# Kernel tuning notes

Measured on AMD Instinct MI355X. Metric: run time of the kernel, lower is better.

The kernel has to match this reference:

```python
import jax, jax.numpy as jnp
import numpy as np
import math

D_MODEL, N_HEADS, D_FF = 512, 8, 2048
B, S = 2, 2048
EPS = 1e-6


def _layernorm(x, g, b):
    mu = jnp.mean(x, axis=-1, keepdims=True)
    var = jnp.mean((x - mu) ** 2, axis=-1, keepdims=True)
    return (x - mu) * jax.lax.rsqrt(var + EPS) * g + b


def setup_inputs() -> dict:
    key = jax.random.key(0)
    ks = jax.random.split(key, 16)
    sd = 1.0 / math.sqrt(D_MODEL)
    return {
        "x": jax.random.normal(ks[0], (B, S, D_MODEL), jnp.float32),
        "sensor_weights": jax.random.uniform(ks[1], (B, S, 4), jnp.float32),
        "mask": jnp.ones((1, 1, S, S), jnp.int32),
        "Wq": jax.random.normal(ks[2], (D_MODEL, D_MODEL), jnp.float32) * sd,
        "Wk": jax.random.normal(ks[3], (D_MODEL, D_MODEL), jnp.float32) * sd,
        "Wv": jax.random.normal(ks[4], (D_MODEL, D_MODEL), jnp.float32) * sd,
        "Wo": jax.random.normal(ks[5], (D_MODEL, D_MODEL), jnp.float32) * sd,
        "bo": jnp.zeros((D_MODEL,), jnp.float32),
        "sensor_attention": jnp.ones((N_HEADS, 4), jnp.float32),  # init = ones
        "temporal_bias": jax.random.normal(ks[6], (1, N_HEADS, 1, 1), jnp.float32) * 0.02,
        "ln1_g": jnp.ones((D_MODEL,), jnp.float32),
        "ln1_b": jnp.zeros((D_MODEL,), jnp.float32),
        "ln2_g": jnp.ones((D_MODEL,), jnp.float32),
        "ln2_b": jnp.zeros((D_MODEL,), jnp.float32),
        "W1": jax.random.normal(ks[7], (D_MODEL, D_FF), jnp.float32) * sd,
        "b1": jnp.zeros((D_FF,), jnp.float32),
        "W2": jax.random.normal(ks[8], (D_FF, D_MODEL), jnp.float32) * (1.0 / math.sqrt(D_FF)),
        "b2": jnp.zeros((D_MODEL,), jnp.float32),
    }


def reference(x, sensor_weights, mask, Wq, Wk, Wv, Wo, bo, sensor_attention,
              temporal_bias, ln1_g, ln1_b, ln2_g, ln2_b, W1, b1, W2, b2):
    b, s, d = x.shape
    h = temporal_bias.shape[1]
    dk = d // h
    scale = math.sqrt(dk)

    # [b, h, s, dk]
    q = (x @ Wq).reshape(b, s, h, dk).transpose(0, 2, 1, 3)
    k = (x @ Wk).reshape(b, s, h, dk).transpose(0, 2, 1, 3)
    v = (x @ Wv).reshape(b, s, h, dk).transpose(0, 2, 1, 3)

    scores = jnp.einsum('bhqd,bhkd->bhqk', q, k) / scale  # [b,h,s,s]
    scores = scores + temporal_bias
    # sensor bias: [h,4] x [b,s,4] -> [b,h,s], added per query row
    sensor_bias = jnp.einsum('hf,bsf->bhs', sensor_attention, sensor_weights)
    scores = scores + sensor_bias[..., None]
    scores = jnp.where(mask == 0, jnp.asarray(-1e9, scores.dtype), scores)

    attn = jax.nn.softmax(scores, axis=-1)
    ctx = jnp.einsum('bhqk,bhkd->bhqd', attn, v)
    ctx = ctx.transpose(0, 2, 1, 3).reshape(b, s, d)
    attn_out = ctx @ Wo + bo

    x1 = _layernorm(x + attn_out, ln1_g, ln1_b)
    ff = jax.nn.gelu(x1 @ W1 + b1, approximate=False) @ W2 + b2
    x2 = _layernorm(x1 + ff, ln2_g, ln2_b)
    return x2, attn
```

## Files before the change

### kernel.cpp

```cpp
#include <hip/hip_runtime.h>
#include <cstdint>
#include <cstddef>

#define S_LEN 2048
#define DM 512
#define NH 8
#define DK 64
#define DFF 2048
#define BATCH 2
#define NROWS (BATCH*S_LEN)
#define BHN (BATCH*NH)

#define MASKED_L2 (-1.4426950408889634e9f)
#define QSCALE 0.18033688011112042f

typedef __attribute__((ext_vector_type(8))) _Float16 f16x8;
typedef __attribute__((ext_vector_type(4))) float f32x4;

#define MFMA(a,b,c) __builtin_amdgcn_mfma_f32_16x16x32_f16(a,b,c,0,0,0)

__device__ __forceinline__ unsigned short f2h(float x){
  union{ _Float16 h; unsigned short u; } c; c.h = (_Float16)x; return c.u;
}
__device__ __forceinline__ int sw64(int r, int c){
  return r*64 + ((((c>>3) ^ r) & 7)<<3) + (c&7);
}
__device__ __forceinline__ int sw32(int r, int c){
  return r*32 + ((((c>>3) ^ r) & 3)<<3) + (c&7);
}

__global__ __launch_bounds__(256) void prep_kernel(
    const float* __restrict__ x, const int* __restrict__ mask,
    const float* __restrict__ Wq, const float* __restrict__ Wk,
    const float* __restrict__ Wv, const float* __restrict__ Wo,
    const float* __restrict__ W1, const float* __restrict__ W2,
    unsigned short* __restrict__ xb,
    unsigned short* __restrict__ wqT, unsigned short* __restrict__ wkT,
    unsigned short* __restrict__ wvT, unsigned short* __restrict__ woT,
    unsigned short* __restrict__ w1T, unsigned short* __restrict__ w2T,
    unsigned* __restrict__ maskw)
{
  const int z = blockIdx.y;
  const int t = blockIdx.x;
  const int tid = threadIdx.x;
  if (z < 6){
    const float* W; unsigned short* WT; int K, N;
    switch(z){
      case 0: W=Wq; WT=wqT; K=512;  N=512;  break;
      case 1: W=Wk; WT=wkT; K=512;  N=512;  break;
      case 2: W=Wv; WT=wvT; K=512;  N=512;  break;
      case 3: W=Wo; WT=woT; K=512;  N=512;  break;
      case 4: W=W1; WT=w1T; K=512;  N=2048; break;
      default:W=W2; WT=w2T; K=2048; N=512;  break;
    }
    const int ntiles = N>>5, ktiles = K>>5;
    if (t >= ntiles*ktiles) return;
    const int kt = t / ntiles, nt = t - kt*ntiles;
    __shared__ float tile[32][33];
    const int tx = tid & 31, ty = tid >> 5;
    #pragma unroll
    for (int i=0;i<4;i++){
      int r = ty + i*8;
      tile[r][tx] = W[(size_t)(kt*32 + r)*N + nt*32 + tx];
    }
    __syncthreads();
    #pragma unroll
    for (int i=0;i<4;i++){
      int r = ty + i*8;
      WT[(size_t)(nt*32 + r)*K + kt*32 + tx] = f2h(tile[tx][r]);
    }
  } else if (z == 6){
    size_t base = (size_t)t*2048 + (size_t)tid*8;
    float4 a = *(const float4*)(x + base);
    float4 b = *(const float4*)(x + base + 4);
    union{ unsigned short h[8]; uint4 v; } pk;
    pk.h[0]=f2h(a.x); pk.h[1]=f2h(a.y); pk.h[2]=f2h(a.z); pk.h[3]=f2h(a.w);
    pk.h[4]=f2h(b.x); pk.h[5]=f2h(b.y); pk.h[6]=f2h(b.z); pk.h[7]=f2h(b.w);
    *(uint4*)(xb + base) = pk.v;
  } else {
    if (t >= 512) return;
    const int gid = t*256 + tid;
    const int row = gid >> 6, w = gid & 63;
    const int4* mp = (const int4*)(mask + (size_t)row*2048 + w*32);
    unsigned word = 0;
    #pragma unroll
    for (int j=0;j<8;j++){
      int4 v = mp[j];
      word |= (unsigned)(v.x!=0) << (j*4+0);
      word |= (unsigned)(v.y!=0) << (j*4+1);
      word |= (unsigned)(v.z!=0) << (j*4+2);
      word |= (unsigned)(v.w!=0) << (j*4+3);
    }
    maskw[gid] = word;
  }
}

template<int KD, int EPI>
__global__ __launch_bounds__(256) void gemm_kernel(
    const unsigned short* __restrict__ A,
    const unsigned short* __restrict__ BT0,
    const unsigned short* __restrict__ BT1,
    const unsigned short* __restrict__ BT2,
    const float* __restrict__ bias,
    const float* __restrict__ resid,
    float* __restrict__ outf,
    unsigned short* __restrict__ ob0,
    unsigned short* __restrict__ ob1,
    unsigned short* __restrict__ ob2)
{
  const unsigned short* BT = BT0;
  unsigned short* outb = ob0;
  float scale = 1.0f;
  if (EPI == 0){
    const int z = blockIdx.z;
    if (z == 0) scale = QSCALE;
    else if (z == 1){ BT = BT1; outb = ob1; }
    else            { BT = BT2; outb = ob2; }
  }
  const int m0 = blockIdx.x*64, n0 = blockIdx.y*64;
  const int tid = threadIdx.x;
  const int wid = tid>>6, l = tid&63, quad = l>>4, lc = l&15;
  const int wm = wid&1, wn = wid>>1;
  __shared__ __align__(16) unsigned short As[2][64*32];
  __shared__ __align__(16) unsigned short Bs[2][64*32];
  const int sr = tid>>2, sc = (tid&3)*8;
  const unsigned short* Ap = A  + (size_t)(m0+sr)*KD + sc;
  const unsigned short* Bp = BT + (size_t)(n0+sr)*KD + sc;
  {
    uint4 va = *(const uint4*)Ap;
    uint4 vb = *(const uint4*)Bp;
    *(uint4*)&As[0][sw32(sr,sc)] = va;
    *(uint4*)&Bs[0][sw32(sr,sc)] = vb;
  }
  f32x4 acc00={0,0,0,0}, acc01={0,0,0,0}, acc10={0,0,0,0}, acc11={0,0,0,0};
  const int ar0 = wm*32 + lc, ar1 = wm*32 + 16 + lc;
  const int br0 = wn*32 + lc, br1 = wn*32 + 16 + lc;
  __syncthreads();
  constexpr int NK = KD/32;
  for (int kk=0; kk<NK; kk++){
    const int cur = kk & 1;
    if (kk+1 < NK){
      uint4 va = *(const uint4*)(Ap + (size_t)(kk+1)*32);
      uint4 vb = *(const uint4*)(Bp + (size_t)(kk+1)*32);
      *(uint4*)&As[cur^1][sw32(sr,sc)] = va;
      *(uint4*)&Bs[cur^1][sw32(sr,sc)] = vb;
    }
    f16x8 a0 = *(const f16x8*)&As[cur][sw32(ar0, quad*8)];
    f16x8 a1 = *(const f16x8*)&As[cur][sw32(ar1, quad*8)];
    f16x8 b0 = *(const f16x8*)&Bs[cur][sw32(br0, quad*8)];
    f16x8 b1 = *(const f16x8*)&Bs[cur][sw32(br1, quad*8)];
    acc00 = MFMA(a0,b0,acc00);
    acc01 = MFMA(a0,b1,acc01);
    acc10 = MFMA(a1,b0,acc10);
    acc11 = MFMA(a1,b1,acc11);
    __syncthreads();
  }
  f32x4 accs[2][2] = {{acc00,acc01},{acc10,acc11}};
  #pragma unroll
  for (int mt=0;mt<2;mt++){
    #pragma unroll
    for (int nt=0;nt<2;nt++){
      f32x4 v = accs[mt][nt];
      const int col  = n0 + wn*32 + nt*16 + lc;
      const int row0 = m0 + wm*32 + mt*16 + quad*4;
      #pragma unroll
      for (int r=0;r<4;r++){
        const int row = row0 + r;
        const float val = v[r];
        if (EPI == 0){
          const int h = col>>6, d = col&63, b = row>>11, s = row&2047;
          outb[(((size_t)(b*NH + h))*S_LEN + s)*DK + d] = f2h(val*scale);
        } else if (EPI == 1){
          const size_t idx = (size_t)row*DM + col;
          outf[idx] = val + bias[col] + resid[idx];
        } else {
          const float xx = val + bias[col];
          const float gg = 0.5f*xx*(1.0f + erff(xx*0.70710678118654752f));
          outb[(size_t)row*DFF + col] = f2h(gg);
        }
      }
    }
  }
}

__global__ __launch_bounds__(256) void kml_kernel(
    const unsigned short* __restrict__ qw,
    const unsigned short* __restrict__ kw,
    const unsigned* __restrict__ maskw,
    float* __restrict__ m_out, float* __restrict__ li_out)
{
  const int bh = blockIdx.y, q0 = blockIdx.x*64;
  const int tid = threadIdx.x, wid = tid>>6, l = tid&63, quad = l>>4, lc = l&15;
  __shared__ __align__(16) unsigned short Qs[64*64];
  __shared__ __align__(16) unsigned short Ks[2][64*64];
  const unsigned short* qbase = qw + ((size_t)bh*S_LEN + q0)*DK;
  const unsigned short* kbase = kw + (size_t)bh*S_LEN*DK;
  #pragma unroll
  for (int i=0;i<2;i++){
    const int idx = tid + i*256, r = idx>>3, c0 = (idx&7)*8;
    *(uint4*)&Qs[sw64(r,c0)]    = *(const uint4*)(qbase + (size_t)r*DK + c0);
    *(uint4*)&Ks[0][sw64(r,c0)] = *(const uint4*)(kbase + (size_t)r*DK + c0);
  }
  __syncthreads();
  f16x8 aQ0, aQ1;
  {
    const int r = wid*16 + lc;
    aQ0 = *(const f16x8*)&Qs[sw64(r, quad*8)];
    aQ1 = *(const f16x8*)&Qs[sw64(r, 32 + quad*8)];
  }
  float m[4]  = {-3e38f,-3e38f,-3e38f,-3e38f};
  float ls[4] = {0.f,0.f,0.f,0.f};
  const int rowb = q0 + wid*16 + quad*4;
  for (int c=0;c<32;c++){
    const int cur = c & 1;
    if (c+1 < 32){
      #pragma unroll
      for (int i=0;i<2;i++){
        const int idx = tid + i*256, r = idx>>3, c0 = (idx&7)*8;
        *(uint4*)&Ks[cur^1][sw64(r,c0)] =
          *(const uint4*)(kbase + ((size_t)(c+1)*64 + r)*DK + c0);
      }
    }
    uint2 mw[4];
    #pragma unroll
    for (int r=0;r<4;r++)
      mw[r] = *(const uint2*)(maskw + (size_t)(rowb+r)*64 + c*2);
    float sv[4][4];
    #pragma unroll
    for (int nt=0; nt<4; nt++){
      f16x8 b0 = *(const f16x8*)&Ks[cur][sw64(nt*16+lc, quad*8)];
      f16x8 b1 = *(const f16x8*)&Ks[cur][sw64(nt*16+lc, 32+quad*8)];
      f32x4 s = {0,0,0,0};
      s = MFMA(aQ0, b0, s);
      s = MFMA(aQ1, b1, s);
      const int sh = (nt&1)*16 + lc;
      #pragma unroll
      for (int r=0;r<4;r++){
        const unsigned w = (nt<2) ? mw[r].x : mw[r].y;
        sv[nt][r] = ((w>>sh)&1u) ? s[r] : MASKED_L2;
      }
    }
    #pragma unroll
    for (int r=0;r<4;r++){
      const float mc = fmaxf(fmaxf(sv[0][r],sv[1][r]), fmaxf(sv[2][r],sv[3][r]));
      const float m2 = fmaxf(m[r], mc);
      ls[r] = ls[r]*__builtin_exp2f(m[r]-m2)
            + __builtin_exp2f(sv[0][r]-m2) + __builtin_exp2f(sv[1][r]-m2)
            + __builtin_exp2f(sv[2][r]-m2) + __builtin_exp2f(sv[3][r]-m2);
      m[r] = m2;
    }
    __syncthreads();
  }
  #pragma unroll
  for (int o=1;o<16;o<<=1){
    #pragma unroll
    for (int r=0;r<4;r++){
      const float mo = __shfl_xor(m[r], o, 64);
      const float lo = __shfl_xor(ls[r], o, 64);
      const float m2 = fmaxf(m[r], mo);
      ls[r] = ls[r]*__builtin_exp2f(m[r]-m2) + lo*__builtin_exp2f(mo-m2);
      m[r] = m2;
    }
  }
  if (lc == 0){
    const size_t rowg = (size_t)bh*S_LEN + rowb;
    #pragma unroll
    for (int r=0;r<4;r++){
      m_out[rowg+r]  = m[r];
      li_out[rowg+r] = 1.0f/ls[r];
    }
  }
}

__global__ __launch_bounds__(256) void kattn_kernel(
    const unsigned short* __restrict__ qw,
    const unsigned short* __restrict__ kw,
    const unsigned short* __restrict__ vw,
    const unsigned* __restrict__ maskw,
    const float* __restrict__ m_in,
    const float* __restrict__ li_in,
    float* __restrict__ attn,
    unsigned short* __restrict__ ctx)
{
  const int bh = blockIdx.y, q0 = blockIdx.x*64;
  const int tid = threadIdx.x, wid = tid>>6, l = tid&63, quad = l>>4, lc = l&15;
  __shared__ __align__(16) unsigned short Qs[64*64];
  __shared__ __align__(16) unsigned short Ks[2][64*64];
  __shared__ __align__(16) unsigned short Vs[2][64*64];
  __shared__ __align__(16) unsigned short Ps[4][16*64];
  const unsigned short* qbase = qw + ((size_t)bh*S_LEN + q0)*DK;
  const unsigned short* kbase = kw + (size_t)bh*S_LEN*DK;
  const unsigned short* vbase = vw + (size_t)bh*S_LEN*DK;
  #pragma unroll
  for (int i=0;i<2;i++){
    const int idx = tid + i*256, r = idx>>3, c0 = (idx&7)*8;
    *(uint4*)&Qs[sw64(r,c0)]    = *(const uint4*)(qbase + (size_t)r*DK + c0);
    *(uint4*)&Ks[0][sw64(r,c0)] = *(const uint4*)(kbase + (size_t)r*DK + c0);
    union { uint4 u; unsigned short h[8]; } U;
    U.u = *(const uint4*)(vbase + (size_t)r*DK + c0);
    #pragma unroll
    for (int j=0;j<8;j++) Vs[0][sw64(c0+j, r)] = U.h[j];
  }
  __syncthreads();
  f16x8 aQ0, aQ1;
  {
    const int r = wid*16 + lc;
    aQ0 = *(const f16x8*)&Qs[sw64(r, quad*8)];
    aQ1 = *(const f16x8*)&Qs[sw64(r, 32 + quad*8)];
  }
  const int rowb = q0 + wid*16 + quad*4;
  float mr[4], li[4];
  #pragma unroll
  for (int r=0;r<4;r++){
    mr[r] = m_in[(size_t)bh*S_LEN + rowb + r];
    li[r] = li_in[(size_t)bh*S_LEN + rowb + r];
  }
  f32x4 O0={0,0,0,0}, O1={0,0,0,0}, O2={0,0,0,0}, O3={0,0,0,0};
  float* attnbase = attn + (size_t)bh*S_LEN*S_LEN;
  unsigned short* myP = &Ps[wid][0];
  for (int c=0;c<32;c++){
    const int cur = c & 1;
    if (c+1 < 32){
      #pragma unroll
      for (int i=0;i<2;i++){
        const int idx = tid + i*256, r = idx>>3, c0 = (idx&7)*8;
        *(uint4*)&Ks[cur^1][sw64(r,c0)] =
          *(const uint4*)(kbase + ((size_t)(c+1)*64 + r)*DK + c0);
        union { uint4 u; unsigned short h[8]; } U;
        U.u = *(const uint4*)(vbase + ((size_t)(c+1)*64 + r)*DK + c0);
        #pragma unroll
        for (int j=0;j<8;j++) Vs[cur^1][sw64(c0+j, r)] = U.h[j];
      }
    }
    uint2 mw[4];
    #pragma unroll
    for (int r=0;r<4;r++)
      mw[r] = *(const uint2*)(maskw + (size_t)(rowb+r)*64 + c*2);
    #pragma unroll
    for (int nt=0; nt<4; nt++){
      f16x8 b0 = *(const f16x8*)&Ks[cur][sw64(nt*16+lc, quad*8)];
      f16x8 b1 = *(const f16x8*)&Ks[cur][sw64(nt*16+lc, 32+quad*8)];
      f32x4 s = {0,0,0,0};
      s = MFMA(aQ0, b0, s);
      s = MFMA(aQ1, b1, s);
      const int sh = (nt&1)*16 + lc;
      #pragma unroll
      for (int r=0;r<4;r++){
        const unsigned w = (nt<2) ? mw[r].x : mw[r].y;
        const float se = ((w>>sh)&1u) ? s[r] : MASKED_L2;
        const float p  = __builtin_exp2f(se - mr[r]) * li[r];
        __builtin_nontemporal_store(p,
          attnbase + (size_t)(rowb+r)*S_LEN + (size_t)c*64 + nt*16 + lc);
        myP[sw64(quad*4+r, nt*16+lc)] = f2h(p);
      }
    }
    #pragma unroll
    for (int ks=0; ks<2; ks++){
      f16x8 aP = *(const f16x8*)&myP[sw64(lc, ks*32 + quad*8)];
      f16x8 v0 = *(const f16x8*)&Vs[cur][sw64( 0+lc, ks*32+quad*8)];
      f16x8 v1 = *(const f16x8*)&Vs[cur][sw64(16+lc, ks*32+quad*8)];
      f16x8 v2 = *(const f16x8*)&Vs[cur][sw64(32+lc, ks*32+quad*8)];
      f16x8 v3 = *(const f16x8*)&Vs[cur][sw64(48+lc, ks*32+quad*8)];
      O0 = MFMA(aP, v0, O0);
      O1 = MFMA(aP, v1, O1);
      O2 = MFMA(aP, v2, O2);
      O3 = MFMA(aP, v3, O3);
    }
    __syncthreads();
  }
  const int b = bh>>3, h = bh&7;
  f32x4 Os[4] = {O0,O1,O2,O3};
  #pragma unroll
  for (int nt=0; nt<4; nt++){
    #pragma unroll
    for (int r=0;r<4;r++){
      ctx[((size_t)b*S_LEN + rowb + r)*DM + h*DK + nt*16 + lc] = f2h(Os[nt][r]);
    }
  }
}

__global__ __launch_bounds__(256) void ln_kernel(
    const float* __restrict__ in, const float* __restrict__ g,
    const float* __restrict__ b, float* __restrict__ outf,
    unsigned short* __restrict__ outb)
{
  const int row = blockIdx.x*4 + (threadIdx.x>>6);
  const int l = threadIdx.x & 63;
  const float* p = in + (size_t)row*DM + l*8;
  float4 v0 = *(const float4*)p;
  float4 v1 = *(const float4*)(p+4);
  float vals[8] = {v0.x,v0.y,v0.z,v0.w,v1.x,v1.y,v1.z,v1.w};
  float s = 0.f, q = 0.f;
  #pragma unroll
  for (int j=0;j<8;j++){ s += vals[j]; q += vals[j]*vals[j]; }
  #pragma unroll
  for (int o=1;o<64;o<<=1){ s += __shfl_xor(s,o,64); q += __shfl_xor(q,o,64); }
  const float mu = s*(1.0f/DM);
  const float var = q*(1.0f/DM) - mu*mu;
  const float rs = rsqrtf(var + 1e-6f);
  const float* gp = g + l*8;
  const float* bp = b + l*8;
  float4 g0 = *(const float4*)gp, g1 = *(const float4*)(gp+4);
  float4 bb0 = *(const float4*)bp, bb1 = *(const float4*)(bp+4);
  float gv[8] = {g0.x,g0.y,g0.z,g0.w,g1.x,g1.y,g1.z,g1.w};
  float bv[8] = {bb0.x,bb0.y,bb0.z,bb0.w,bb1.x,bb1.y,bb1.z,bb1.w};
  float ov[8];
  #pragma unroll
  for (int j=0;j<8;j++) ov[j] = (vals[j]-mu)*rs*gv[j] + bv[j];
  float* op = outf + (size_t)row*DM + l*8;
  *(float4*)op     = make_float4(ov[0],ov[1],ov[2],ov[3]);
  *(float4*)(op+4) = make_float4(ov[4],ov[5],ov[6],ov[7]);
  if (outb){
    union{ unsigned short h[8]; uint4 v; } pk;
    #pragma unroll
    for (int j=0;j<8;j++) pk.h[j] = f2h(ov[j]);
    *(uint4*)(outb + (size_t)row*DM + l*8) = pk.v;
  }
}

extern "C" void kernel_launch(void* const* d_in, const int* in_sizes, int n_in,
                              void* d_out, int out_size, void* d_ws, size_t ws_size,
                              hipStream_t stream)
{
  const float* x    = (const float*)d_in[0];
  const int*   mask = (const int*)d_in[2];
  const float* Wq   = (const float*)d_in[3];
  const float* Wk   = (const float*)d_in[4];
  const float* Wv   = (const float*)d_in[5];
  const float* Wo   = (const float*)d_in[6];
  const float* bo   = (const float*)d_in[7];
  const float* ln1g = (const float*)d_in[10];
  const float* ln1b = (const float*)d_in[11];
  const float* ln2g = (const float*)d_in[12];
  const float* ln2b = (const float*)d_in[13];
  const float* W1   = (const float*)d_in[14];
  const float* b1   = (const float*)d_in[15];
  const float* W2   = (const float*)d_in[16];
  const float* b2   = (const float*)d_in[17];

  float* x2_out   = (float*)d_out;
  float* attn_out = x2_out + (size_t)NROWS*DM;

  char* p = (char*)d_ws;
  auto alloc = [&](size_t bytes)->char*{
    char* r = p; p += (bytes + 255) & ~(size_t)255; return r;
  };
  unsigned short* xb   = (unsigned short*)alloc((size_t)NROWS*DM*2);
  unsigned short* wqT  = (unsigned short*)alloc(512*512*2);
  unsigned short* wkT  = (unsigned short*)alloc(512*512*2);
  unsigned short* wvT  = (unsigned short*)alloc(512*512*2);
  unsigned short* woT  = (unsigned short*)alloc(512*512*2);
  unsigned short* w1T  = (unsigned short*)alloc(2048*512*2);
  unsigned short* w2T  = (unsigned short*)alloc(512*2048*2);
  unsigned short* q_ws = (unsigned short*)alloc((size_t)BHN*S_LEN*DK*2);
  unsigned short* k_ws = (unsigned short*)alloc((size_t)BHN*S_LEN*DK*2);
  unsigned short* v_ws = (unsigned short*)alloc((size_t)BHN*S_LEN*DK*2);
  unsigned*       maskw= (unsigned*)alloc((size_t)S_LEN*64*4);
  float*          m_ws = (float*)alloc((size_t)BHN*S_LEN*4);
  float*          li_ws= (float*)alloc((size_t)BHN*S_LEN*4);
  unsigned short* ctxb = (unsigned short*)alloc((size_t)NROWS*DM*2);
  float*          yv   = (float*)alloc((size_t)NROWS*DM*4);
  float*          x1f  = (float*)alloc((size_t)NROWS*DM*4);
  unsigned short* x1b  = (unsigned short*)alloc((size_t)NROWS*DM*2);
  unsigned short* hb   = (unsigned short*)alloc((size_t)NROWS*DFF*2);
  float*          zv   = (float*)alloc((size_t)NROWS*DM*4);

  prep_kernel<<<dim3(1024,8), 256, 0, stream>>>(
      x, mask, Wq, Wk, Wv, Wo, W1, W2,
      xb, wqT, wkT, wvT, woT, w1T, w2T, maskw);

  gemm_kernel<512,0><<<dim3(64,8,3), 256, 0, stream>>>(
      xb, wqT, wkT, wvT, nullptr, nullptr, nullptr, q_ws, k_ws, v_ws);

  kml_kernel<<<dim3(32,16), 256, 0, stream>>>(q_ws, k_ws, maskw, m_ws, li_ws);

  kattn_kernel<<<dim3(32,16), 256, 0, stream>>>(
      q_ws, k_ws, v_ws, maskw, m_ws, li_ws, attn_out, ctxb);

  gemm_kernel<512,1><<<dim3(64,8), 256, 0, stream>>>(
      ctxb, woT, nullptr, nullptr, bo, x, yv, nullptr, nullptr, nullptr);

  ln_kernel<<<1024, 256, 0, stream>>>(yv, ln1g, ln1b, x1f, x1b);

  gemm_kernel<512,2><<<dim3(64,32), 256, 0, stream>>>(
      x1b, w1T, nullptr, nullptr, b1, nullptr, nullptr, hb, nullptr, nullptr);

  gemm_kernel<2048,1><<<dim3(64,8), 256, 0, stream>>>(
      hb, w2T, nullptr, nullptr, b2, x1f, zv, nullptr, nullptr, nullptr);

  ln_kernel<<<1024, 256, 0, stream>>>(zv, ln2g, ln2b, x2_out, nullptr);

  (void)in_sizes; (void)n_in; (void)out_size; (void)ws_size;
}
```

Measured before the change: 542.7 us.

## Fuse attention passes, add direct-to-LDS GEMM with larger tiles, pre-transpose V

The two attention kernels (row max/sum pass and probability/context pass) become one kernel. It computes the softmax statistics first, then recomputes the scores to write the attention matrix and the context, and it reads K and a pre-transposed V straight from global memory instead of staging them in shared memory. The GEMMs are replaced by a templated kernel with larger tiles that loads global data directly into LDS, and Q/K/V come from one concatenated weight matrix. This cuts launches and shared-memory traffic, at the cost of a single-buffered GEMM pipeline with no overlap, unswizzled LDS reads that may hit bank conflicts, and an extra V transpose kernel.

```diff
diff --git a/kernel.cpp b/kernel.cpp
--- a/kernel.cpp
+++ b/kernel.cpp
@@ -25,8 +25,11 @@
 __device__ __forceinline__ int sw64(int r, int c){
   return r*64 + ((((c>>3) ^ r) & 7)<<3) + (c&7);
 }
-__device__ __forceinline__ int sw32(int r, int c){
-  return r*32 + ((((c>>3) ^ r) & 3)<<3) + (c&7);
+
+typedef const __attribute__((address_space(1))) uint32_t* gas1;
+typedef __attribute__((address_space(3))) uint32_t* las3;
+__device__ __forceinline__ void gl_lds16(const unsigned short* g, unsigned short* l){
+  __builtin_amdgcn_global_load_lds((gas1)(const void*)g, (las3)(void*)l, 16, 0, 0);
 }
 
 __global__ __launch_bounds__(256) void prep_kernel(
@@ -35,9 +38,8 @@
     const float* __restrict__ Wv, const float* __restrict__ Wo,
     const float* __restrict__ W1, const float* __restrict__ W2,
     unsigned short* __restrict__ xb,
-    unsigned short* __restrict__ wqT, unsigned short* __restrict__ wkT,
-    unsigned short* __restrict__ wvT, unsigned short* __restrict__ woT,
-    unsigned short* __restrict__ w1T, unsigned short* __restrict__ w2T,
+    unsigned short* __restrict__ wqkvT, unsigned short* __restrict__ woT,
+    unsigned short* __restrict__ w1T,   unsigned short* __restrict__ w2T,
     unsigned* __restrict__ maskw)
 {
   const int z = blockIdx.y;
@@ -46,12 +48,12 @@
   if (z < 6){
     const float* W; unsigned short* WT; int K, N;
     switch(z){
-      case 0: W=Wq; WT=wqT; K=512;  N=512;  break;
-      case 1: W=Wk; WT=wkT; K=512;  N=512;  break;
-      case 2: W=Wv; WT=wvT; K=512;  N=512;  break;
-      case 3: W=Wo; WT=woT; K=512;  N=512;  break;
-      case 4: W=W1; WT=w1T; K=512;  N=2048; break;
-      default:W=W2; WT=w2T; K=2048; N=512;  break;
+      case 0: W=Wq; WT=wqkvT;            K=512;  N=512;  break;
+      case 1: W=Wk; WT=wqkvT+512*512;    K=512;  N=512;  break;
+      case 2: W=Wv; WT=wqkvT+2*512*512;  K=512;  N=512;  break;
+      case 3: W=Wo; WT=woT;              K=512;  N=512;  break;
+      case 4: W=W1; WT=w1T;              K=512;  N=2048; break;
+      default:W=W2; WT=w2T;              K=2048; N=512;  break;
     }
     const int ntiles = N>>5, ktiles = K>>5;
     if (t >= ntiles*ktiles) return;
@@ -95,130 +97,156 @@
   }
 }
 
-template<int KD, int EPI>
-__global__ __launch_bounds__(256) void gemm_kernel(
+template<int BM, int BN, int KD, int EPI>
+__global__ __launch_bounds__(256) void gemm2(
     const unsigned short* __restrict__ A,
-    const unsigned short* __restrict__ BT0,
-    const unsigned short* __restrict__ BT1,
-    const unsigned short* __restrict__ BT2,
+    const unsigned short* __restrict__ BT,
     const float* __restrict__ bias,
     const float* __restrict__ resid,
     float* __restrict__ outf,
-    unsigned short* __restrict__ ob0,
-    unsigned short* __restrict__ ob1,
-    unsigned short* __restrict__ ob2)
-{
-  const unsigned short* BT = BT0;
-  unsigned short* outb = ob0;
-  float scale = 1.0f;
-  if (EPI == 0){
-    const int z = blockIdx.z;
-    if (z == 0) scale = QSCALE;
-    else if (z == 1){ BT = BT1; outb = ob1; }
-    else            { BT = BT2; outb = ob2; }
-  }
-  const int m0 = blockIdx.x*64, n0 = blockIdx.y*64;
-  const int tid = threadIdx.x;
-  const int wid = tid>>6, l = tid&63, quad = l>>4, lc = l&15;
-  const int wm = wid&1, wn = wid>>1;
-  __shared__ __align__(16) unsigned short As[2][64*32];
-  __shared__ __align__(16) unsigned short Bs[2][64*32];
-  const int sr = tid>>2, sc = (tid&3)*8;
-  const unsigned short* Ap = A  + (size_t)(m0+sr)*KD + sc;
-  const unsigned short* Bp = BT + (size_t)(n0+sr)*KD + sc;
-  {
-    uint4 va = *(const uint4*)Ap;
-    uint4 vb = *(const uint4*)Bp;
-    *(uint4*)&As[0][sw32(sr,sc)] = va;
-    *(uint4*)&Bs[0][sw32(sr,sc)] = vb;
-  }
-  f32x4 acc00={0,0,0,0}, acc01={0,0,0,0}, acc10={0,0,0,0}, acc11={0,0,0,0};
-  const int ar0 = wm*32 + lc, ar1 = wm*32 + 16 + lc;
-  const int br0 = wn*32 + lc, br1 = wn*32 + 16 + lc;
-  __syncthreads();
-  constexpr int NK = KD/32;
-  for (int kk=0; kk<NK; kk++){
-    const int cur = kk & 1;
-    if (kk+1 < NK){
-      uint4 va = *(const uint4*)(Ap + (size_t)(kk+1)*32);
-      uint4 vb = *(const uint4*)(Bp + (size_t)(kk+1)*32);
-      *(uint4*)&As[cur^1][sw32(sr,sc)] = va;
-      *(uint4*)&Bs[cur^1][sw32(sr,sc)] = vb;
-    }
-    f16x8 a0 = *(const f16x8*)&As[cur][sw32(ar0, quad*8)];
-    f16x8 a1 = *(const f16x8*)&As[cur][sw32(ar1, quad*8)];
-    f16x8 b0 = *(const f16x8*)&Bs[cur][sw32(br0, quad*8)];
-    f16x8 b1 = *(const f16x8*)&Bs[cur][sw32(br1, quad*8)];
-    acc00 = MFMA(a0,b0,acc00);
-    acc01 = MFMA(a0,b1,acc01);
-    acc10 = MFMA(a1,b0,acc10);
-    acc11 = MFMA(a1,b1,acc11);
+    unsigned short* __restrict__ outq,
+    unsigned short* __restrict__ outk,
+    unsigned short* __restrict__ outv)
+{
+  constexpr int WGM = (BM >= 128) ? 2 : 1;
+  constexpr int WGN = 4 / WGM;
+  constexpr int WTM = BM / WGM;
+  constexpr int WTN = BN / WGN;
+  constexpr int MT = WTM / 16;
+  constexpr int NT = WTN / 16;
+  constexpr int NKS = KD / 32;
+  constexpr int AISS = (BM*4)/256;
+  constexpr int BISS = (BN*4)/256;
+  __shared__ __align__(16) unsigned short As[BM*32];
+  __shared__ __align__(16) unsigned short Bs[BN*32];
+  const int tid = threadIdx.x, wid = tid>>6, l = tid&63, quad = l>>4, lc = l&15;
+  const int m0 = blockIdx.x*BM, n0 = blockIdx.y*BN;
+  const int wm = (WGM==2) ? (wid&1) : 0;
+  const int wn = (WGM==2) ? (wid>>1) : wid;
+  f32x4 acc[MT][NT] = {};
+  for (int kk=0; kk<NKS; kk++){
+    #pragma unroll
+    for (int i=0;i<AISS;i++){
+      const int ch = i*256 + tid;
+      gl_lds16(A + (size_t)(m0 + (ch>>2))*KD + kk*32 + (ch&3)*8,
+               &As[(i*256 + wid*64)*8]);
+    }
+    #pragma unroll
+    for (int i=0;i<BISS;i++){
+      const int ch = i*256 + tid;
+      gl_lds16(BT + (size_t)(n0 + (ch>>2))*KD + kk*32 + (ch&3)*8,
+               &Bs[(i*256 + wid*64)*8]);
+    }
     __syncthreads();
-  }
-  f32x4 accs[2][2] = {{acc00,acc01},{acc10,acc11}};
-  #pragma unroll
-  for (int mt=0;mt<2;mt++){
-    #pragma unroll
-    for (int nt=0;nt<2;nt++){
-      f32x4 v = accs[mt][nt];
-      const int col  = n0 + wn*32 + nt*16 + lc;
-      const int row0 = m0 + wm*32 + mt*16 + quad*4;
+    f16x8 af[MT], bf[NT];
+    #pragma unroll
+    for (int i=0;i<MT;i++)
+      af[i] = *(const f16x8*)&As[(wm*WTM + i*16 + lc)*32 + quad*8];
+    #pragma unroll
+    for (int j=0;j<NT;j++)
+      bf[j] = *(const f16x8*)&Bs[(wn*WTN + j*16 + lc)*32 + quad*8];
+    #pragma unroll
+    for (int i=0;i<MT;i++)
+      #pragma unroll
+      for (int j=0;j<NT;j++)
+        acc[i][j] = MFMA(af[i], bf[j], acc[i][j]);
+    __syncthreads();
+  }
+  #pragma unroll
+  for (int i=0;i<MT;i++){
+    const int row0 = m0 + wm*WTM + i*16 + quad*4;
+    #pragma unroll
+    for (int j=0;j<NT;j++){
+      const int col = n0 + wn*WTN + j*16 + lc;
+      f32x4 v = acc[i][j];
       #pragma unroll
       for (int r=0;r<4;r++){
         const int row = row0 + r;
         const float val = v[r];
         if (EPI == 0){
-          const int h = col>>6, d = col&63, b = row>>11, s = row&2047;
-          outb[(((size_t)(b*NH + h))*S_LEN + s)*DK + d] = f2h(val*scale);
+          const int z = col>>9, cw = col&511, h = cw>>6, d = cw&63;
+          const int b = row>>11, s = row&2047;
+          unsigned short* dst = (z==0)?outq:(z==1)?outk:outv;
+          const float sc = (z==0)?QSCALE:1.0f;
+          dst[(((size_t)(b*NH + h))*S_LEN + s)*DK + d] = f2h(val*sc);
         } else if (EPI == 1){
           const size_t idx = (size_t)row*DM + col;
           outf[idx] = val + bias[col] + resid[idx];
         } else {
           const float xx = val + bias[col];
           const float gg = 0.5f*xx*(1.0f + erff(xx*0.70710678118654752f));
-          outb[(size_t)row*DFF + col] = f2h(gg);
+          outq[(size_t)row*DFF + col] = f2h(gg);
         }
       }
     }
   }
 }
 
-__global__ __launch_bounds__(256) void kml_kernel(
+__global__ __launch_bounds__(256) void vtrans_kernel(
+    const unsigned short* __restrict__ v, unsigned short* __restrict__ vt)
+{
+  __shared__ unsigned short t[64][66];
+  const int bh = blockIdx.y, s0 = blockIdx.x*64;
+  const int tid = threadIdx.x;
+  #pragma unroll
+  for (int i=0;i<2;i++){
+    const int idx = tid + i*256;
+    const int row = idx>>3, col = (idx&7)*8;
+    *(uint4*)&t[row][col] =
+      *(const uint4*)(v + ((size_t)bh*S_LEN + s0 + row)*DK + col);
+  }
+  __syncthreads();
+  #pragma unroll
+  for (int i=0;i<2;i++){
+    const int idx = tid + i*256;
+    const int d = idx>>3, sc = (idx&7)*8;
+    union{ unsigned short h[8]; uint4 u; } pk;
+    #pragma unroll
+    for (int j=0;j<8;j++) pk.h[j] = t[sc+j][d];
+    *(uint4*)(vt + ((size_t)bh*DK + d)*S_LEN + s0 + sc) = pk.u;
+  }
+}
+
+__global__ __launch_bounds__(256) void attn_fused(
     const unsigned short* __restrict__ qw,
     const unsigned short* __restrict__ kw,
+    const unsigned short* __restrict__ vt,
     const unsigned* __restrict__ maskw,
-    float* __restrict__ m_out, float* __restrict__ li_out)
-{
-  const int bh = blockIdx.y, q0 = blockIdx.x*64;
+    float* __restrict__ attn,
+    unsigned short* __restrict__ ctx)
+{
+  const int bh = blockIdx.y;
   const int tid = threadIdx.x, wid = tid>>6, l = tid&63, quad = l>>4, lc = l&15;
-  __shared__ __align__(16) unsigned short Qs[64*64];
-  __shared__ __align__(16) unsigned short Ks[2][64*64];
-  const unsigned short* qbase = qw + ((size_t)bh*S_LEN + q0)*DK;
-  const unsigned short* kbase = kw + (size_t)bh*S_LEN*DK;
-  #pragma unroll
-  for (int i=0;i<2;i++){
-    const int idx = tid + i*256, r = idx>>3, c0 = (idx&7)*8;
-    *(uint4*)&Qs[sw64(r,c0)]    = *(const uint4*)(qbase + (size_t)r*DK + c0);
-    *(uint4*)&Ks[0][sw64(r,c0)] = *(const uint4*)(kbase + (size_t)r*DK + c0);
-  }
-  __syncthreads();
-  f16x8 aQ0, aQ1;
-  {
-    const int r = wid*16 + lc;
-    aQ0 = *(const f16x8*)&Qs[sw64(r, quad*8)];
-    aQ1 = *(const f16x8*)&Qs[sw64(r, 32 + quad*8)];
-  }
+  const int q0 = blockIdx.x*64 + wid*16;
+  __shared__ __align__(16) unsigned short Pbuf[4][16*64];
+  unsigned short* myP = Pbuf[wid];
+  const unsigned short* qb = qw + ((size_t)bh*S_LEN + q0)*DK;
+  const unsigned short* kb = kw + (size_t)bh*S_LEN*DK;
+  const unsigned short* vb = vt + (size_t)bh*DK*S_LEN;
+  const f16x8 aQ0 = *(const f16x8*)(qb + (size_t)lc*DK + quad*8);
+  const f16x8 aQ1 = *(const f16x8*)(qb + (size_t)lc*DK + 32 + quad*8);
+  const int rowb = q0 + quad*4;
+
   float m[4]  = {-3e38f,-3e38f,-3e38f,-3e38f};
   float ls[4] = {0.f,0.f,0.f,0.f};
-  const int rowb = q0 + wid*16 + quad*4;
+
+  f16x8 nb0[4], nb1[4];
+  #pragma unroll
+  for (int nt=0;nt<4;nt++){
+    const unsigned short* kp = kb + (size_t)(nt*16+lc)*DK;
+    nb0[nt] = *(const f16x8*)(kp + quad*8);
+    nb1[nt] = *(const f16x8*)(kp + 32 + quad*8);
+  }
   for (int c=0;c<32;c++){
-    const int cur = c & 1;
+    f16x8 cb0[4], cb1[4];
+    #pragma unroll
+    for (int nt=0;nt<4;nt++){ cb0[nt]=nb0[nt]; cb1[nt]=nb1[nt]; }
     if (c+1 < 32){
       #pragma unroll
-      for (int i=0;i<2;i++){
-        const int idx = tid + i*256, r = idx>>3, c0 = (idx&7)*8;
-        *(uint4*)&Ks[cur^1][sw64(r,c0)] =
-          *(const uint4*)(kbase + ((size_t)(c+1)*64 + r)*DK + c0);
+      for (int nt=0;nt<4;nt++){
+        const unsigned short* kp = kb + (size_t)((c+1)*64 + nt*16+lc)*DK;
+        nb0[nt] = *(const f16x8*)(kp + quad*8);
+        nb1[nt] = *(const f16x8*)(kp + 32 + quad*8);
       }
     }
     uint2 mw[4];
@@ -227,12 +255,10 @@
       mw[r] = *(const uint2*)(maskw + (size_t)(rowb+r)*64 + c*2);
     float sv[4][4];
     #pragma unroll
-    for (int nt=0; nt<4; nt++){
-      f16x8 b0 = *(const f16x8*)&Ks[cur][sw64(nt*16+lc, quad*8)];
-      f16x8 b1 = *(const f16x8*)&Ks[cur][sw64(nt*16+lc, 32+quad*8)];
+    for (int nt=0;nt<4;nt++){
       f32x4 s = {0,0,0,0};
-      s = MFMA(aQ0, b0, s);
-      s = MFMA(aQ1, b1, s);
+      s = MFMA(aQ0, cb0[nt], s);
+      s = MFMA(aQ1, cb1[nt], s);
       const int sh = (nt&1)*16 + lc;
       #pragma unroll
       for (int r=0;r<4;r++){
@@ -249,7 +275,6 @@
             + __builtin_exp2f(sv[2][r]-m2) + __builtin_exp2f(sv[3][r]-m2);
       m[r] = m2;
     }
-    __syncthreads();
   }
   #pragma unroll
   for (int o=1;o<16;o<<=1){
@@ -262,84 +287,22 @@
       m[r] = m2;
     }
   }
-  if (lc == 0){
-    const size_t rowg = (size_t)bh*S_LEN + rowb;
-    #pragma unroll
-    for (int r=0;r<4;r++){
-      m_out[rowg+r]  = m[r];
-      li_out[rowg+r] = 1.0f/ls[r];
-    }
-  }
-}
-
-__global__ __launch_bounds__(256) void kattn_kernel(
-    const unsigned short* __restrict__ qw,
-    const unsigned short* __restrict__ kw,
-    const unsigned short* __restrict__ vw,
-    const unsigned* __restrict__ maskw,
-    const float* __restrict__ m_in,
-    const float* __restrict__ li_in,
-    float* __restrict__ attn,
-    unsigned short* __restrict__ ctx)
-{
-  const int bh = blockIdx.y, q0 = blockIdx.x*64;
-  const int tid = threadIdx.x, wid = tid>>6, l = tid&63, quad = l>>4, lc = l&15;
-  __shared__ __align__(16) unsigned short Qs[64*64];
-  __shared__ __align__(16) unsigned short Ks[2][64*64];
-  __shared__ __align__(16) unsigned short Vs[2][64*64];
-  __shared__ __align__(16) unsigned short Ps[4][16*64];
-  const unsigned short* qbase = qw + ((size_t)bh*S_LEN + q0)*DK;
-  const unsigned short* kbase = kw + (size_t)bh*S_LEN*DK;
-  const unsigned short* vbase = vw + (size_t)bh*S_LEN*DK;
-  #pragma unroll
-  for (int i=0;i<2;i++){
-    const int idx = tid + i*256, r = idx>>3, c0 = (idx&7)*8;
-    *(uint4*)&Qs[sw64(r,c0)]    = *(const uint4*)(qbase + (size_t)r*DK + c0);
-    *(uint4*)&Ks[0][sw64(r,c0)] = *(const uint4*)(kbase + (size_t)r*DK + c0);
-    union { uint4 u; unsigned short h[8]; } U;
-    U.u = *(const uint4*)(vbase + (size_t)r*DK + c0);
-    #pragma unroll
-    for (int j=0;j<8;j++) Vs[0][sw64(c0+j, r)] = U.h[j];
-  }
-  __syncthreads();
-  f16x8 aQ0, aQ1;
-  {
-    const int r = wid*16 + lc;
-    aQ0 = *(const f16x8*)&Qs[sw64(r, quad*8)];
-    aQ1 = *(const f16x8*)&Qs[sw64(r, 32 + quad*8)];
-  }
-  const int rowb = q0 + wid*16 + quad*4;
-  float mr[4], li[4];
-  #pragma unroll
-  for (int r=0;r<4;r++){
-    mr[r] = m_in[(size_t)bh*S_LEN + rowb + r];
-    li[r] = li_in[(size_t)bh*S_LEN + rowb + r];
-  }
-  f32x4 O0={0,0,0,0}, O1={0,0,0,0}, O2={0,0,0,0}, O3={0,0,0,0};
-  float* attnbase = attn + (size_t)bh*S_LEN*S_LEN;
-  unsigned short* myP = &Ps[wid][0];
+  float li[4];
+  #pragma unroll
+  for (int r=0;r<4;r++) li[r] = 1.0f/ls[r];
+
+  f32x4 O[4] = {{0,0,0,0},{0,0,0,0},{0,0,0,0},{0,0,0,0}};
+  float* ab = attn + (size_t)bh*S_LEN*S_LEN;
   for (int c=0;c<32;c++){
-    const int cur = c & 1;
-    if (c+1 < 32){
-      #pragma unroll
-      for (int i=0;i<2;i++){
-        const int idx = tid + i*256, r = idx>>3, c0 = (idx&7)*8;
-        *(uint4*)&Ks[cur^1][sw64(r,c0)] =
-          *(const uint4*)(kbase + ((size_t)(c+1)*64 + r)*DK + c0);
-        union { uint4 u; unsigned short h[8]; } U;
-        U.u = *(const uint4*)(vbase + ((size_t)(c+1)*64 + r)*DK + c0);
-        #pragma unroll
-        for (int j=0;j<8;j++) Vs[cur^1][sw64(c0+j, r)] = U.h[j];
-      }
-    }
     uint2 mw[4];
     #pragma unroll
     for (int r=0;r<4;r++)
       mw[r] = *(const uint2*)(maskw + (size_t)(rowb+r)*64 + c*2);
     #pragma unroll
-    for (int nt=0; nt<4; nt++){
-      f16x8 b0 = *(const f16x8*)&Ks[cur][sw64(nt*16+lc, quad*8)];
-      f16x8 b1 = *(const f16x8*)&Ks[cur][sw64(nt*16+lc, 32+quad*8)];
+    for (int nt=0;nt<4;nt++){
+      const unsigned short* kp = kb + (size_t)(c*64 + nt*16+lc)*DK;
+      f16x8 b0 = *(const f16x8*)(kp + quad*8);
+      f16x8 b1 = *(const f16x8*)(kp + 32 + quad*8);
       f32x4 s = {0,0,0,0};
       s = MFMA(aQ0, b0, s);
       s = MFMA(aQ1, b1, s);
@@ -348,34 +311,28 @@
       for (int r=0;r<4;r++){
         const unsigned w = (nt<2) ? mw[r].x : mw[r].y;
         const float se = ((w>>sh)&1u) ? s[r] : MASKED_L2;
-        const float p  = __builtin_exp2f(se - mr[r]) * li[r];
+        const float p  = __builtin_exp2f(se - m[r]) * li[r];
         __builtin_nontemporal_store(p,
-          attnbase + (size_t)(rowb+r)*S_LEN + (size_t)c*64 + nt*16 + lc);
+          ab + (size_t)(rowb+r)*S_LEN + (size_t)c*64 + nt*16 + lc);
         myP[sw64(quad*4+r, nt*16+lc)] = f2h(p);
       }
     }
     #pragma unroll
-    for (int ks=0; ks<2; ks++){
+    for (int ks=0;ks<2;ks++){
       f16x8 aP = *(const f16x8*)&myP[sw64(lc, ks*32 + quad*8)];
-      f16x8 v0 = *(const f16x8*)&Vs[cur][sw64( 0+lc, ks*32+quad*8)];
-      f16x8 v1 = *(const f16x8*)&Vs[cur][sw64(16+lc, ks*32+quad*8)];
-      f16x8 v2 = *(const f16x8*)&Vs[cur][sw64(32+lc, ks*32+quad*8)];
-      f16x8 v3 = *(const f16x8*)&Vs[cur][sw64(48+lc, ks*32+quad*8)];
-      O0 = MFMA(aP, v0, O0);
-      O1 = MFMA(aP, v1, O1);
-      O2 = MFMA(aP, v2, O2);
-      O3 = MFMA(aP, v3, O3);
-    }
-    __syncthreads();
+      #pragma unroll
+      for (int dt=0;dt<4;dt++){
+        f16x8 vv = *(const f16x8*)(vb + (size_t)(dt*16+lc)*S_LEN + c*64 + ks*32 + quad*8);
+        O[dt] = MFMA(aP, vv, O[dt]);
+      }
+    }
   }
   const int b = bh>>3, h = bh&7;
-  f32x4 Os[4] = {O0,O1,O2,O3};
-  #pragma unroll
-  for (int nt=0; nt<4; nt++){
-    #pragma unroll
-    for (int r=0;r<4;r++){
-      ctx[((size_t)b*S_LEN + rowb + r)*DM + h*DK + nt*16 + lc] = f2h(Os[nt][r]);
-    }
+  #pragma unroll
+  for (int dt=0;dt<4;dt++){
+    #pragma unroll
+    for (int r=0;r<4;r++)
+      ctx[((size_t)b*S_LEN + rowb + r)*DM + h*DK + dt*16 + lc] = f2h(O[dt][r]);
   }
 }
 
@@ -445,48 +402,45 @@
   auto alloc = [&](size_t bytes)->char*{
     char* r = p; p += (bytes + 255) & ~(size_t)255; return r;
   };
-  unsigned short* xb   = (unsigned short*)alloc((size_t)NROWS*DM*2);
-  unsigned short* wqT  = (unsigned short*)alloc(512*512*2);
-  unsigned short* wkT  = (unsigned short*)alloc(512*512*2);
-  unsigned short* wvT  = (unsigned short*)alloc(512*512*2);
-  unsigned short* woT  = (unsigned short*)alloc(512*512*2);
-  unsigned short* w1T  = (unsigned short*)alloc(2048*512*2);
-  unsigned short* w2T  = (unsigned short*)alloc(512*2048*2);
-  unsigned short* q_ws = (unsigned short*)alloc((size_t)BHN*S_LEN*DK*2);
-  unsigned short* k_ws = (unsigned short*)alloc((size_t)BHN*S_LEN*DK*2);
-  unsigned short* v_ws = (unsigned short*)alloc((size_t)BHN*S_LEN*DK*2);
-  unsigned*       maskw= (unsigned*)alloc((size_t)S_LEN*64*4);
-  float*          m_ws = (float*)alloc((size_t)BHN*S_LEN*4);
-  float*          li_ws= (float*)alloc((size_t)BHN*S_LEN*4);
-  unsigned short* ctxb = (unsigned short*)alloc((size_t)NROWS*DM*2);
-  float*          yv   = (float*)alloc((size_t)NROWS*DM*4);
-  float*          x1f  = (float*)alloc((size_t)NROWS*DM*4);
-  unsigned short* x1b  = (unsigned short*)alloc((size_t)NROWS*DM*2);
-  unsigned short* hb   = (unsigned short*)alloc((size_t)NROWS*DFF*2);
-  float*          zv   = (float*)alloc((size_t)NROWS*DM*4);
+  unsigned short* xb    = (unsigned short*)alloc((size_t)NROWS*DM*2);
+  unsigned short* wqkvT = (unsigned short*)alloc((size_t)3*512*512*2);
+  unsigned short* woT   = (unsigned short*)alloc(512*512*2);
+  unsigned short* w1T   = (unsigned short*)alloc(2048*512*2);
+  unsigned short* w2T   = (unsigned short*)alloc(512*2048*2);
+  unsigned short* q_ws  = (unsigned short*)alloc((size_t)BHN*S_LEN*DK*2);
+  unsigned short* k_ws  = (unsigned short*)alloc((size_t)BHN*S_LEN*DK*2);
+  unsigned short* v_ws  = (unsigned short*)alloc((size_t)BHN*S_LEN*DK*2);
+  unsigned short* vT    = (unsigned short*)alloc((size_t)BHN*DK*S_LEN*2);
+  unsigned*       maskw = (unsigned*)alloc((size_t)S_LEN*64*4);
+  unsigned short* ctxb  = (unsigned short*)alloc((size_t)NROWS*DM*2);
+  float*          yv    = (float*)alloc((size_t)NROWS*DM*4);
+  float*          x1f   = (float*)alloc((size_t)NROWS*DM*4);
+  unsigned short* x1b   = (unsigned short*)alloc((size_t)NROWS*DM*2);
+  unsigned short* hb    = (unsigned short*)alloc((size_t)NROWS*DFF*2);
+  float*          zv    = (float*)alloc((size_t)NROWS*DM*4);
 
   prep_kernel<<<dim3(1024,8), 256, 0, stream>>>(
       x, mask, Wq, Wk, Wv, Wo, W1, W2,
-      xb, wqT, wkT, wvT, woT, w1T, w2T, maskw);
-
-  gemm_kernel<512,0><<<dim3(64,8,3), 256, 0, stream>>>(
-      xb, wqT, wkT, wvT, nullptr, nullptr, nullptr, q_ws, k_ws, v_ws);
-
-  kml_kernel<<<dim3(32,16), 256, 0, stream>>>(q_ws, k_ws, maskw, m_ws, li_ws);
-
-  kattn_kernel<<<dim3(32,16), 256, 0, stream>>>(
-      q_ws, k_ws, v_ws, maskw, m_ws, li_ws, attn_out, ctxb);
-
-  gemm_kernel<512,1><<<dim3(64,8), 256, 0, stream>>>(
-      ctxb, woT, nullptr, nullptr, bo, x, yv, nullptr, nullptr, nullptr);
+      xb, wqkvT, woT, w1T, w2T, maskw);
+
+  gemm2<128,128,512,0><<<dim3(32,12), 256, 0, stream>>>(
+      xb, wqkvT, nullptr, nullptr, nullptr, q_ws, k_ws, v_ws);
+
+  vtrans_kernel<<<dim3(32,16), 256, 0, stream>>>(v_ws, vT);
+
+  attn_fused<<<dim3(32,16), 256, 0, stream>>>(
+      q_ws, k_ws, vT, maskw, attn_out, ctxb);
+
+  gemm2<64,128,512,1><<<dim3(64,4), 256, 0, stream>>>(
+      ctxb, woT, bo, x, yv, nullptr, nullptr, nullptr);
 
   ln_kernel<<<1024, 256, 0, stream>>>(yv, ln1g, ln1b, x1f, x1b);
 
-  gemm_kernel<512,2><<<dim3(64,32), 256, 0, stream>>>(
-      x1b, w1T, nullptr, nullptr, b1, nullptr, nullptr, hb, nullptr, nullptr);
-
-  gemm_kernel<2048,1><<<dim3(64,8), 256, 0, stream>>>(
-      hb, w2T, nullptr, nullptr, b2, x1f, zv, nullptr, nullptr, nullptr);
+  gemm2<128,128,512,2><<<dim3(32,16), 256, 0, stream>>>(
+      x1b, w1T, b1, nullptr, nullptr, hb, nullptr, nullptr);
+
+  gemm2<64,128,2048,1><<<dim3(64,4), 256, 0, stream>>>(
+      hb, w2T, b2, x1f, zv, nullptr, nullptr, nullptr);
 
   ln_kernel<<<1024, 256, 0, stream>>>(zv, ln2g, ln2b, x2_out, nullptr);
 
```

Result: slower. 597.8 us (+10.2%).
